# Kernel optimization log

Hardware: AMD Instinct MI355X
Metric: run time of the kernel (lower is better)

Reference implementation:

```python
import jax, jax.numpy as jnp
import numpy as np

D_MODEL = 512
N_EXPERTS = 8
TOPK = 2
D_FF = D_MODEL * 4
LB_WEIGHT = 0.01


def setup_inputs() -> dict:
    key = jax.random.key(0)
    k_x, k_g, k_w1, k_v1, k_w2 = jax.random.split(key, 5)
    B, L = 4, 2048
    x = jax.random.normal(k_x, (B, L, D_MODEL), dtype=jnp.float32)
    # nn.Linear gate weight, init std=0.01, shape [n_experts, d_model]
    gate_w = 0.01 * jax.random.normal(k_g, (N_EXPERTS, D_MODEL), dtype=jnp.float32)
    # kaiming_normal_ fan_in / relu: std = sqrt(2 / fan_in); fan_in is last dim
    std1 = np.sqrt(2.0 / D_MODEL).astype(np.float32)
    std2 = np.sqrt(2.0 / D_FF).astype(np.float32)
    W1 = std1 * jax.random.normal(k_w1, (N_EXPERTS, D_FF, D_MODEL), dtype=jnp.float32)
    V1 = std1 * jax.random.normal(k_v1, (N_EXPERTS, D_FF, D_MODEL), dtype=jnp.float32)
    W2 = std2 * jax.random.normal(k_w2, (N_EXPERTS, D_MODEL, D_FF), dtype=jnp.float32)
    return {"x": x, "gate_w": gate_w, "W1": W1, "V1": V1, "W2": W2}


def reference(x, gate_w, W1, V1, W2):
    B, L, D = x.shape
    T = B * L
    x_flat = x.reshape(T, D)

    # --- gating ---
    logits = x_flat @ gate_w.T                      # [T, E]
    probs = jax.nn.softmax(logits, axis=-1)         # [T, E]
    scores, indices = jax.lax.top_k(probs, TOPK)    # [T, K] each

    # combine weights: [T, E]; top-k indices per token are distinct
    oh = jax.nn.one_hot(indices, N_EXPERTS, dtype=x.dtype)    # [T, K, E]
    combine = jnp.einsum('tke,tk->te', oh, scores)            # [T, E]

    # load-balancing aux loss
    load = oh.sum(axis=(0, 1))                      # [E] tokens routed per expert
    f = load / T
    P = probs.mean(axis=0)                          # [E]
    aux_loss = N_EXPERTS * jnp.sum(f * P) * LB_WEIGHT

    # --- SwiGLU experts (dense over experts, masked combine) ---
    h = jnp.einsum('td,efd->etf', x_flat, W1)       # [E, T, d_ff]
    v = jnp.einsum('td,efd->etf', x_flat, V1)       # [E, T, d_ff]
    y = jnp.einsum('etf,edf->etd', jax.nn.silu(h) * v, W2)   # [E, T, D]

    out = jnp.einsum('te,etd->td', combine, y).reshape(B, L, D)
    return out, aux_loss
```

## Files before the change

kernel.cpp:

```cpp
#include <hip/hip_runtime.h>
#include <hip/hip_bf16.h>
#include <stdint.h>

#define D_MODEL 512
#define N_EXP 8
#define D_FF 2048
#define NTOK 8192
#define TM 256
#define MAX_TILES 72
#define NEPAD (MAX_TILES*TM)
#define BK 64

typedef __attribute__((ext_vector_type(8))) short short8;
typedef __attribute__((ext_vector_type(4))) float f32x4;

struct Ctrl {
  int cnt[8];
  int cursor[8];
  int offpad[16];
  int ntiles;
  int pad[3];
  int texp[MAX_TILES];
};

__device__ __forceinline__ unsigned short f2bf(float f){
  unsigned u = __float_as_uint(f);
  u += 0x7FFFu + ((u>>16)&1u);
  return (unsigned short)(u>>16);
}
__device__ __forceinline__ float bf2f(unsigned short v){
  return __uint_as_float(((unsigned)v)<<16);
}

__device__ __forceinline__ short8 pack8(float4 a, float4 b){
  short8 o;
  o[0]=(short)f2bf(a.x); o[1]=(short)f2bf(a.y); o[2]=(short)f2bf(a.z); o[3]=(short)f2bf(a.w);
  o[4]=(short)f2bf(b.x); o[5]=(short)f2bf(b.y); o[6]=(short)f2bf(b.z); o[7]=(short)f2bf(b.w);
  return o;
}

__device__ __forceinline__ void gload16(const void* g, void* l){
  __builtin_amdgcn_global_load_lds((const __attribute__((address_space(1))) unsigned int*)g,
                                   (__attribute__((address_space(3))) unsigned int*)l, 16, 0, 0);
}

#define SBAR0 __builtin_amdgcn_sched_barrier(0)
#define BAR   do{ SBAR0; __builtin_amdgcn_s_barrier(); SBAR0; }while(0)
#define LGKM0 do{ asm volatile("s_waitcnt lgkmcnt(0)" ::: "memory"); SBAR0; }while(0)
#define VM(N) do{ asm volatile("s_waitcnt vmcnt(" #N ")" ::: "memory"); SBAR0; }while(0)

__global__ void __launch_bounds__(256)
prep_kernel(const float* __restrict__ x, const float* __restrict__ gw,
            const float* __restrict__ W1, const float* __restrict__ V1, const float* __restrict__ W2,
            unsigned short* __restrict__ W1b, unsigned short* __restrict__ V1b, unsigned short* __restrict__ W2d,
            int* __restrict__ tok_e, float* __restrict__ tok_s,
            Ctrl* __restrict__ c, float* __restrict__ Pbins,
            unsigned short* __restrict__ Xb){
  __shared__ float gws[N_EXP*D_MODEL];
  __shared__ float pblk[4][8];
  __shared__ int cblk[8];
  int bid = blockIdx.x;
  int tid = threadIdx.x;
  if(bid >= 2048){
    int j = bid - 2048;
    const float* src = (j<4096) ? W1 : (j<8192 ? V1 : W2);
    unsigned short* dst = (j<4096) ? W1b : (j<8192 ? V1b : W2d);
    int i = (j & 4095)*2048 + tid*8;
    float4 a = *(const float4*)(src+i);
    float4 b = *(const float4*)(src+i+4);
    *(short8*)(dst+i) = pack8(a,b);
    return;
  }
  for(int i=tid; i<N_EXP*D_MODEL; i+=256) gws[i]=gw[i];
  if(tid<8) cblk[tid]=0;
  __syncthreads();
  int wave = tid>>6, lane = tid&63;
  int t = bid*4 + wave;
  const float* xr = x + (size_t)t*D_MODEL + lane*8;
  float4 xa = *(const float4*)xr;
  float4 xb = *(const float4*)(xr+4);
  *(short8*)(Xb + (size_t)t*D_MODEL + lane*8) = pack8(xa,xb);
  float le[8];
  #pragma unroll
  for(int e=0;e<8;e++){
    const float* g = gws + e*D_MODEL + lane*8;
    float4 ga = *(const float4*)g;
    float4 gb = *(const float4*)(g+4);
    le[e] = xa.x*ga.x + xa.y*ga.y + xa.z*ga.z + xa.w*ga.w
          + xb.x*gb.x + xb.y*gb.y + xb.z*gb.z + xb.w*gb.w;
  }
  #pragma unroll
  for(int e=0;e<8;e++){
    float v = le[e];
    #pragma unroll
    for(int off=1; off<64; off<<=1) v += __shfl_xor(v, off);
    le[e]=v;
  }
  float mx = le[0];
  #pragma unroll
  for(int e=1;e<8;e++) mx = fmaxf(mx, le[e]);
  float p[8], s=0.f;
  #pragma unroll
  for(int e=0;e<8;e++){ p[e]=__expf(le[e]-mx); s+=p[e]; }
  float inv = 1.0f/s;
  #pragma unroll
  for(int e=0;e<8;e++) p[e]*=inv;
  int e0=0; float s0=p[0];
  #pragma unroll
  for(int e=1;e<8;e++) if(p[e]>s0){e0=e;s0=p[e];}
  int e1=-1; float s1=-1.f;
  #pragma unroll
  for(int e=0;e<8;e++) if(e!=e0 && p[e]>s1){e1=e;s1=p[e];}
  if(lane==0){
    tok_e[2*t]=e0; tok_e[2*t+1]=e1;
    tok_s[2*t]=s0; tok_s[2*t+1]=s1;
    atomicAdd(&cblk[e0],1); atomicAdd(&cblk[e1],1);
    #pragma unroll
    for(int e=0;e<8;e++) pblk[wave][e]=p[e];
  }
  __syncthreads();
  if(tid<8){
    atomicAdd(&c->cnt[tid], cblk[tid]);
    atomicAdd(&Pbins[(bid&63)*8 + tid],
              pblk[0][tid]+pblk[1][tid]+pblk[2][tid]+pblk[3][tid]);
  }
}

__global__ void __launch_bounds__(256)
cvt_kernel(const float* __restrict__ src, unsigned short* __restrict__ dst, int n){
  int i = (blockIdx.x*256 + threadIdx.x)*8;
  if(i >= n) return;
  float4 a = *(const float4*)(src+i);
  float4 b = *(const float4*)(src+i+4);
  *(short8*)(dst+i) = pack8(a,b);
}

__global__ void __launch_bounds__(256)
scan_kernel(Ctrl* __restrict__ c, const float* __restrict__ Pbins, float* __restrict__ out){
  __shared__ float pred[4][8];
  int tid = threadIdx.x;
  float v = Pbins[tid] + Pbins[tid+256];
  v += __shfl_xor(v, 8);
  v += __shfl_xor(v, 16);
  v += __shfl_xor(v, 32);
  if((tid&63)<8) pred[tid>>6][tid&7] = v;
  __syncthreads();
  if(tid==0){
    int o=0, tc=0;
    float aux=0.f;
    for(int e=0;e<8;e++){
      float tot = pred[0][e]+pred[1][e]+pred[2][e]+pred[3][e];
      c->offpad[e]=o;
      int nt = (c->cnt[e]+TM-1)/TM;
      for(int i=0;i<nt;i++) c->texp[tc++]=e;
      o += nt*TM;
      c->cursor[e]=0;
      aux += ((float)c->cnt[e]/(float)NTOK) * (tot/(float)NTOK);
    }
    c->offpad[8]=o;
    c->ntiles=tc;
    out[(size_t)NTOK*D_MODEL] = 8.0f*0.01f*aux;
  }
}

__global__ void __launch_bounds__(256)
scatter_kernel(const int* __restrict__ tok_e, const float* __restrict__ tok_s,
               Ctrl* __restrict__ c, int* __restrict__ etok, float* __restrict__ escl,
               int* __restrict__ pos){
  int t = blockIdx.x*256 + threadIdx.x;
  if(t >= NTOK) return;
  #pragma unroll
  for(int k=0;k<2;k++){
    int e = tok_e[2*t+k];
    int p = atomicAdd(&c->cursor[e],1);
    int i = c->offpad[e]+p;
    etok[i]=t; escl[i]=tok_s[2*t+k];
    pos[2*t+k]=i;
  }
}

__global__ void __launch_bounds__(512,2)
expA_kernel(const unsigned short* __restrict__ Xb, const unsigned short* __restrict__ W1b,
            const unsigned short* __restrict__ V1b, const int* __restrict__ etok,
            const Ctrl* __restrict__ c, unsigned short* __restrict__ G){
  __shared__ short8 As[2][2048];
  __shared__ short8 Bs[2][2048];
  int bid = blockIdx.x;
  int chunk = bid & 7;
  int w_in = bid >> 3;
  int fb = w_in / 9;
  int tile = chunk*9 + (w_in - fb*9);
  int fbase = fb * 128;
  if(tile >= c->ntiles) return;
  int e = c->texp[tile];
  int base = tile*TM;
  int tid = threadIdx.x;

  int r0 = tid>>3;
  int cs = (tid&7) ^ (r0&7);
  int t0 = etok[base + r0];
  int t1 = etok[base + 64 + r0];
  int t2 = etok[base + 128 + r0];
  int t3 = etok[base + 192 + r0];
  const unsigned short* sA0 = Xb + (size_t)t0*D_MODEL + cs*8;
  const unsigned short* sA1 = Xb + (size_t)t1*D_MODEL + cs*8;
  const unsigned short* sA2 = Xb + (size_t)t2*D_MODEL + cs*8;
  const unsigned short* sA3 = Xb + (size_t)t3*D_MODEL + cs*8;
  const unsigned short* WE = W1b + (size_t)e*(D_FF*D_MODEL);
  const unsigned short* VE = V1b + (size_t)e*(D_FF*D_MODEL);
  const unsigned short* sB0 = WE + (size_t)(fbase+r0)*D_MODEL + cs*8;
  const unsigned short* sB1 = WE + (size_t)(fbase+64+r0)*D_MODEL + cs*8;
  const unsigned short* sB2 = VE + (size_t)(fbase+r0)*D_MODEL + cs*8;
  const unsigned short* sB3 = VE + (size_t)(fbase+64+r0)*D_MODEL + cs*8;
  int w64 = tid & ~63;

  int lane = tid&63, lrow = lane&15, lk = lane>>4;
  int wid = tid>>6, wr = wid>>2, wc = wid&3;
  int sw = lrow&7;
  int ch0 = lk ^ sw;
  int ch1 = (4+lk) ^ sw;

  f32x4 hacc[8][2], vacc[8][2];
  #pragma unroll
  for(int mi=0;mi<8;mi++)
    #pragma unroll
    for(int nj=0;nj<2;nj++){
      hacc[mi][nj]=(f32x4){0.f,0.f,0.f,0.f};
      vacc[mi][nj]=(f32x4){0.f,0.f,0.f,0.f};
    }

  auto ST_A0 = [&](int b, int kt){ size_t o=(size_t)kt*BK; gload16(sA0+o, &As[b][w64]);      gload16(sA1+o, &As[b][512+w64]); };
  auto ST_A1 = [&](int b, int kt){ size_t o=(size_t)kt*BK; gload16(sA2+o, &As[b][1024+w64]); gload16(sA3+o, &As[b][1536+w64]); };
  auto ST_W  = [&](int b, int kt){ size_t o=(size_t)kt*BK; gload16(sB0+o, &Bs[b][w64]);      gload16(sB1+o, &Bs[b][512+w64]); };
  auto ST_V  = [&](int b, int kt){ size_t o=(size_t)kt*BK; gload16(sB2+o, &Bs[b][1024+w64]); gload16(sB3+o, &Bs[b][1536+w64]); };

  ST_A0(0,0); ST_A1(0,0); ST_W(0,0); ST_V(0,0);
  ST_W(1,1); ST_V(1,1); ST_A0(1,1);
  VM(6);
  BAR;

  short8 alo[4][2], ahi[4][2], bw[2][2], bv[2][2];

  #pragma unroll
  for(int k=0;k<8;k++){
    const int cur = k&1, nxt = cur^1;
    #pragma unroll
    for(int j=0;j<4;j++){
      int s = (wr*128 + j*16 + lrow)*8;
      alo[j][0] = As[cur][s + ch0];
      alo[j][1] = As[cur][s + ch1];
    }
    #pragma unroll
    for(int nj=0;nj<2;nj++){
      int s = (wc*32 + nj*16 + lrow)*8;
      bw[nj][0] = Bs[cur][s + ch0];
      bw[nj][1] = Bs[cur][s + ch1];
    }
    if(k<7) ST_A1(nxt, k+1);
    BAR; LGKM0;
    __builtin_amdgcn_s_setprio(1);
    #pragma unroll
    for(int j=0;j<4;j++)
      #pragma unroll
      for(int nj=0;nj<2;nj++){
        hacc[j][nj] = __builtin_amdgcn_mfma_f32_16x16x32_bf16(alo[j][0], bw[nj][0], hacc[j][nj],0,0,0);
        hacc[j][nj] = __builtin_amdgcn_mfma_f32_16x16x32_bf16(alo[j][1], bw[nj][1], hacc[j][nj],0,0,0);
      }
    __builtin_amdgcn_s_setprio(0);
    BAR;
    #pragma unroll
    for(int nj=0;nj<2;nj++){
      int s = 1024 + (wc*32 + nj*16 + lrow)*8;
      bv[nj][0] = Bs[cur][s + ch0];
      bv[nj][1] = Bs[cur][s + ch1];
    }
    if(k<6) ST_W(cur, k+2);
    BAR; LGKM0;
    __builtin_amdgcn_s_setprio(1);
    #pragma unroll
    for(int j=0;j<4;j++)
      #pragma unroll
      for(int nj=0;nj<2;nj++){
        vacc[j][nj] = __builtin_amdgcn_mfma_f32_16x16x32_bf16(alo[j][0], bv[nj][0], vacc[j][nj],0,0,0);
        vacc[j][nj] = __builtin_amdgcn_mfma_f32_16x16x32_bf16(alo[j][1], bv[nj][1], vacc[j][nj],0,0,0);
      }
    __builtin_amdgcn_s_setprio(0);
    BAR;
    #pragma unroll
    for(int j=0;j<4;j++){
      int s = (wr*128 + 64 + j*16 + lrow)*8;
      ahi[j][0] = As[cur][s + ch0];
      ahi[j][1] = As[cur][s + ch1];
    }
    if(k<6) ST_V(cur, k+2);
    BAR; LGKM0;
    __builtin_amdgcn_s_setprio(1);
    #pragma unroll
    for(int j=0;j<4;j++)
      #pragma unroll
      for(int nj=0;nj<2;nj++){
        vacc[4+j][nj] = __builtin_amdgcn_mfma_f32_16x16x32_bf16(ahi[j][0], bv[nj][0], vacc[4+j][nj],0,0,0);
        vacc[4+j][nj] = __builtin_amdgcn_mfma_f32_16x16x32_bf16(ahi[j][1], bv[nj][1], vacc[4+j][nj],0,0,0);
      }
    __builtin_amdgcn_s_setprio(0);
    BAR;
    if(k<6) ST_A0(cur, k+2);
    if(k<6){ VM(6); } else { VM(0); }
    BAR;
    __builtin_amdgcn_s_setprio(1);
    #pragma unroll
    for(int j=0;j<4;j++)
      #pragma unroll
      for(int nj=0;nj<2;nj++){
        hacc[4+j][nj] = __builtin_amdgcn_mfma_f32_16x16x32_bf16(ahi[j][0], bw[nj][0], hacc[4+j][nj],0,0,0);
        hacc[4+j][nj] = __builtin_amdgcn_mfma_f32_16x16x32_bf16(ahi[j][1], bw[nj][1], hacc[4+j][nj],0,0,0);
      }
    __builtin_amdgcn_s_setprio(0);
    BAR;
  }

  #pragma unroll
  for(int mi=0;mi<8;mi++){
    int m = base + wr*128 + mi*16 + lk*4;
    #pragma unroll
    for(int nj=0;nj<2;nj++){
      int f = fbase + wc*32 + nj*16 + lrow;
      #pragma unroll
      for(int r=0;r<4;r++){
        float h = hacc[mi][nj][r], vv = vacc[mi][nj][r];
        float g = (h/(1.0f+__expf(-h)))*vv;
        G[(size_t)(m+r)*D_FF + f] = f2bf(g);
      }
    }
  }
}

__global__ void __launch_bounds__(512,2)
expB_kernel(const unsigned short* __restrict__ G, const unsigned short* __restrict__ W2b,
            const Ctrl* __restrict__ c, unsigned short* __restrict__ Ye){
  __shared__ short8 As2[2][2048];
  __shared__ short8 Bs2[2][2048];
  int bid = blockIdx.x;
  int w = (bid & 7)*18 + (bid >> 3);
  int tile = w >> 1;
  int nb = w & 1;
  if(tile >= c->ntiles) return;
  int e = c->texp[tile];
  int base = tile*TM;
  int nbase = nb*256;
  int tid = threadIdx.x;

  int r0 = tid>>3;
  int cs = (tid&7) ^ (r0&7);
  const unsigned short* sA0 = G + (size_t)(base+r0)*D_FF + cs*8;
  const unsigned short* sA1 = G + (size_t)(base+64+r0)*D_FF + cs*8;
  const unsigned short* sA2 = G + (size_t)(base+128+r0)*D_FF + cs*8;
  const unsigned short* sA3 = G + (size_t)(base+192+r0)*D_FF + cs*8;
  const unsigned short* W2E = W2b + (size_t)e*(D_MODEL*D_FF);
  const unsigned short* sB0 = W2E + (size_t)(nbase+r0)*D_FF + cs*8;
  const unsigned short* sB1 = W2E + (size_t)(nbase+64+r0)*D_FF + cs*8;
  const unsigned short* sB2 = W2E + (size_t)(nbase+128+r0)*D_FF + cs*8;
  const unsigned short* sB3 = W2E + (size_t)(nbase+192+r0)*D_FF + cs*8;
  int w64 = tid & ~63;

  int lane = tid&63, lrow = lane&15, lk = lane>>4;
  int wid = tid>>6, wr = wid>>2, wc = wid&3;
  int sw = lrow&7;
  int ch0 = lk ^ sw;
  int ch1 = (4+lk) ^ sw;

  f32x4 acc[8][4];
  #pragma unroll
  for(int mi=0;mi<8;mi++)
    #pragma unroll
    for(int nj=0;nj<4;nj++) acc[mi][nj]=(f32x4){0.f,0.f,0.f,0.f};

  auto ST_A0 = [&](int b, int kt){ size_t o=(size_t)kt*BK; gload16(sA0+o, &As2[b][w64]);      gload16(sA1+o, &As2[b][512+w64]); };
  auto ST_A1 = [&](int b, int kt){ size_t o=(size_t)kt*BK; gload16(sA2+o, &As2[b][1024+w64]); gload16(sA3+o, &As2[b][1536+w64]); };
  auto ST_B0 = [&](int b, int kt){ size_t o=(size_t)kt*BK; gload16(sB0+o, &Bs2[b][w64]);      gload16(sB1+o, &Bs2[b][512+w64]); };
  auto ST_B1 = [&](int b, int kt){ size_t o=(size_t)kt*BK; gload16(sB2+o, &Bs2[b][1024+w64]); gload16(sB3+o, &Bs2[b][1536+w64]); };

  ST_B0(0,0); ST_B1(0,0); ST_A0(0,0); ST_A1(0,0);
  ST_B0(1,1); ST_B1(1,1);
  VM(4);
  BAR;

  short8 alo[4][2], ahi[4][2], bl[2][2], bh[2][2];

  #pragma unroll 2
  for(int k=0;k<32;k++){
    const int cur = k&1, nxt = cur^1;
    #pragma unroll
    for(int j=0;j<4;j++){
      int s = (wr*128 + j*16 + lrow)*8;
      alo[j][0] = As2[cur][s + ch0];
      alo[j][1] = As2[cur][s + ch1];
    }
    #pragma unroll
    for(int nj=0;nj<2;nj++){
      int s = (wc*64 + nj*16 + lrow)*8;
      bl[nj][0] = Bs2[cur][s + ch0];
      bl[nj][1] = Bs2[cur][s + ch1];
    }
    if(k<31) ST_A0(nxt, k+1);
    BAR; LGKM0;
    __builtin_amdgcn_s_setprio(1);
    #pragma unroll
    for(int j=0;j<4;j++)
      #pragma unroll
      for(int nj=0;nj<2;nj++){
        acc[j][nj] = __builtin_amdgcn_mfma_f32_16x16x32_bf16(alo[j][0], bl[nj][0], acc[j][nj],0,0,0);
        acc[j][nj] = __builtin_amdgcn_mfma_f32_16x16x32_bf16(alo[j][1], bl[nj][1], acc[j][nj],0,0,0);
      }
    __builtin_amdgcn_s_setprio(0);
    BAR;
    #pragma unroll
    for(int nj=0;nj<2;nj++){
      int s = (wc*64 + 32 + nj*16 + lrow)*8;
      bh[nj][0] = Bs2[cur][s + ch0];
      bh[nj][1] = Bs2[cur][s + ch1];
    }
    if(k<31) ST_A1(nxt, k+1);
    BAR; LGKM0;
    __builtin_amdgcn_s_setprio(1);
    #pragma unroll
    for(int j=0;j<4;j++)
      #pragma unroll
      for(int nj=0;nj<2;nj++){
        acc[j][2+nj] = __builtin_amdgcn_mfma_f32_16x16x32_bf16(alo[j][0], bh[nj][0], acc[j][2+nj],0,0,0);
        acc[j][2+nj] = __builtin_amdgcn_mfma_f32_16x16x32_bf16(alo[j][1], bh[nj][1], acc[j][2+nj],0,0,0);
      }
    __builtin_amdgcn_s_setprio(0);
    BAR;
    #pragma unroll
    for(int j=0;j<4;j++){
      int s = (wr*128 + 64 + j*16 + lrow)*8;
      ahi[j][0] = As2[cur][s + ch0];
      ahi[j][1] = As2[cur][s + ch1];
    }
    if(k<30) ST_B0(cur, k+2);
    BAR; LGKM0;
    __builtin_amdgcn_s_setprio(1);
    #pragma unroll
    for(int j=0;j<4;j++)
      #pragma unroll
      for(int nj=0;nj<2;nj++){
        acc[4+j][2+nj] = __builtin_amdgcn_mfma_f32_16x16x32_bf16(ahi[j][0], bh[nj][0], acc[4+j][2+nj],0,0,0);
        acc[4+j][2+nj] = __builtin_amdgcn_mfma_f32_16x16x32_bf16(ahi[j][1], bh[nj][1], acc[4+j][2+nj],0,0,0);
      }
    __builtin_amdgcn_s_setprio(0);
    BAR;
    if(k<30) ST_B1(cur, k+2);
    if(k<30){ VM(4); } else { VM(0); }
    BAR;
    __builtin_amdgcn_s_setprio(1);
    #pragma unroll
    for(int j=0;j<4;j++)
      #pragma unroll
      for(int nj=0;nj<2;nj++){
        acc[4+j][nj] = __builtin_amdgcn_mfma_f32_16x16x32_bf16(ahi[j][0], bl[nj][0], acc[4+j][nj],0,0,0);
        acc[4+j][nj] = __builtin_amdgcn_mfma_f32_16x16x32_bf16(ahi[j][1], bl[nj][1], acc[4+j][nj],0,0,0);
      }
    __builtin_amdgcn_s_setprio(0);
    BAR;
  }

  #pragma unroll
  for(int mi=0;mi<8;mi++){
    #pragma unroll
    for(int r=0;r<4;r++){
      int m = base + wr*128 + mi*16 + lk*4 + r;
      #pragma unroll
      for(int nj=0;nj<4;nj++){
        int n = nbase + wc*64 + nj*16 + lrow;
        Ye[(size_t)m*D_MODEL + n] = f2bf(acc[mi][nj][r]);
      }
    }
  }
}

__global__ void __launch_bounds__(256)
combine_kernel(const unsigned short* __restrict__ Ye, const int* __restrict__ pos,
               const float* __restrict__ tok_s, float* __restrict__ out){
  int wave = threadIdx.x>>6, lane = threadIdx.x&63;
  int t = blockIdx.x*4 + wave;
  int p0 = pos[2*t], p1 = pos[2*t+1];
  float s0 = tok_s[2*t], s1 = tok_s[2*t+1];
  short8 y0 = *(const short8*)(Ye + (size_t)p0*D_MODEL + lane*8);
  short8 y1 = *(const short8*)(Ye + (size_t)p1*D_MODEL + lane*8);
  float* o = out + (size_t)t*D_MODEL + lane*8;
  float v[8];
  #pragma unroll
  for(int i=0;i<8;i++)
    v[i] = s0*bf2f((unsigned short)y0[i]) + s1*bf2f((unsigned short)y1[i]);
  float4 lo = {v[0],v[1],v[2],v[3]};
  float4 hi = {v[4],v[5],v[6],v[7]};
  *(float4*)o = lo;
  *(float4*)(o+4) = hi;
}

extern "C" void kernel_launch(void* const* d_in, const int* in_sizes, int n_in,
                              void* d_out, int out_size, void* d_ws, size_t ws_size,
                              hipStream_t stream) {
  (void)in_sizes; (void)n_in; (void)out_size;
  const float* x  = (const float*)d_in[0];
  const float* gw = (const float*)d_in[1];
  const float* W1 = (const float*)d_in[2];
  const float* V1 = (const float*)d_in[3];
  const float* W2 = (const float*)d_in[4];
  float* out = (float*)d_out;

  const size_t WSZ = (size_t)N_EXP*D_FF*D_MODEL;
  const size_t XSZ = (size_t)NTOK*D_MODEL;
  char* ws = (char*)d_ws;
  size_t off = 0;
  unsigned short* W1b = (unsigned short*)(ws+off); off += WSZ*2;
  unsigned short* V1b = (unsigned short*)(ws+off); size_t v1_off = off; off += WSZ*2;
  unsigned short* Xb  = (unsigned short*)(ws+off); off += XSZ*2;
  unsigned short* G   = (unsigned short*)(ws+off); off += (size_t)NEPAD*D_FF*2;
  int*   etok  = (int*)(ws+off);   size_t entry_off = off; off += (size_t)NEPAD*4;
  float* escl  = (float*)(ws+off); off += (size_t)NEPAD*4;
  size_t entry_bytes = off - entry_off;
  int*   pos   = (int*)(ws+off);   off += (size_t)NTOK*2*4;
  int*   tok_e = (int*)(ws+off);   off += (size_t)NTOK*2*4;
  float* tok_s = (float*)(ws+off); off += (size_t)NTOK*2*4;
  float* Pbins = (float*)(ws+off); size_t pb_off = off; off += 512*4;
  Ctrl*  ctrl  = (Ctrl*)(ws+off);  off += sizeof(Ctrl);
  size_t pb_bytes = off - pb_off;
  unsigned short* Ye  = (unsigned short*)(ws+v1_off);
  if(ws_size < off) return;

  unsigned short* W2d = (unsigned short*)(ws+off);
  bool hoistW2 = (ws_size >= off + WSZ*2);
  unsigned short* W2b = hoistW2 ? W2d : W1b;

  hipMemsetAsync(ws+entry_off, 0, entry_bytes, stream);
  hipMemsetAsync(ws+pb_off, 0, pb_bytes, stream);

  int nconv = hoistW2 ? 3 : 2;
  prep_kernel<<<2048 + nconv*4096, 256, 0, stream>>>(x, gw, W1, V1, W2, W1b, V1b, W2d,
                                                     tok_e, tok_s, ctrl, Pbins, Xb);
  scan_kernel<<<1, 256, 0, stream>>>(ctrl, Pbins, out);
  scatter_kernel<<<NTOK/256, 256, 0, stream>>>(tok_e, tok_s, ctrl, etok, escl, pos);

  expA_kernel<<<1152, 512, 0, stream>>>(Xb, W1b, V1b, etok, ctrl, G);
  if(!hoistW2)
    cvt_kernel<<<(int)WSZ/(256*8), 256, 0, stream>>>(W2, W1b, (int)WSZ);
  expB_kernel<<<144, 512, 0, stream>>>(G, W2b, ctrl, Ye);
  combine_kernel<<<NTOK/4, 256, 0, stream>>>(Ye, pos, tok_s, out);
}
```

Baseline: 316.2 us.

## Merge scan into scatter, drop entry memset, restructure GEMM prefetch to one stage per iteration

Folds the single-block scan kernel into the scatter kernel: every block recomputes the padded per-expert offsets locally, and block 0 writes the tile map and the aux loss. The memset of etok/escl is removed, and expA masks token indices with NTOK-1 so that uninitialised padding rows still point at valid memory. In both expert GEMMs the four staggered partial loads per K-step, each with its own barrier, become a single combined prefetch issued mid-iteration, which cuts most of the barriers. Risks: the cursor relies on being zeroed elsewhere, since the scan no longer resets it; the per-expert tile map (texp, ntiles) is now written by block 0 of the same kernel without any cross-block sync; and the new pipeline waits longer on the prefetch.

```diff
diff --git a/kernel.cpp b/kernel.cpp
--- a/kernel.cpp
+++ b/kernel.cpp
@@ -136,46 +136,50 @@
 }
 
 __global__ void __launch_bounds__(256)
-scan_kernel(Ctrl* __restrict__ c, const float* __restrict__ Pbins, float* __restrict__ out){
+scatter_kernel(const int* __restrict__ tok_e, const float* __restrict__ tok_s,
+               Ctrl* __restrict__ c, int* __restrict__ etok, float* __restrict__ escl,
+               int* __restrict__ pos, const float* __restrict__ Pbins, float* __restrict__ out){
+  __shared__ int soff[8];
   __shared__ float pred[4][8];
   int tid = threadIdx.x;
-  float v = Pbins[tid] + Pbins[tid+256];
-  v += __shfl_xor(v, 8);
-  v += __shfl_xor(v, 16);
-  v += __shfl_xor(v, 32);
-  if((tid&63)<8) pred[tid>>6][tid&7] = v;
+  if(tid==0){
+    int o=0;
+    #pragma unroll
+    for(int e=0;e<8;e++){ soff[e]=o; o += ((c->cnt[e]+TM-1)/TM)*TM; }
+  }
   __syncthreads();
-  if(tid==0){
-    int o=0, tc=0;
-    float aux=0.f;
-    for(int e=0;e<8;e++){
-      float tot = pred[0][e]+pred[1][e]+pred[2][e]+pred[3][e];
-      c->offpad[e]=o;
-      int nt = (c->cnt[e]+TM-1)/TM;
-      for(int i=0;i<nt;i++) c->texp[tc++]=e;
-      o += nt*TM;
-      c->cursor[e]=0;
-      aux += ((float)c->cnt[e]/(float)NTOK) * (tot/(float)NTOK);
-    }
-    c->offpad[8]=o;
-    c->ntiles=tc;
-    out[(size_t)NTOK*D_MODEL] = 8.0f*0.01f*aux;
-  }
-}
-
-__global__ void __launch_bounds__(256)
-scatter_kernel(const int* __restrict__ tok_e, const float* __restrict__ tok_s,
-               Ctrl* __restrict__ c, int* __restrict__ etok, float* __restrict__ escl,
-               int* __restrict__ pos){
-  int t = blockIdx.x*256 + threadIdx.x;
-  if(t >= NTOK) return;
+  int t = blockIdx.x*256 + tid;
   #pragma unroll
   for(int k=0;k<2;k++){
     int e = tok_e[2*t+k];
     int p = atomicAdd(&c->cursor[e],1);
-    int i = c->offpad[e]+p;
+    int i = soff[e]+p;
     etok[i]=t; escl[i]=tok_s[2*t+k];
     pos[2*t+k]=i;
+  }
+  if(blockIdx.x==0){
+    float v = Pbins[tid] + Pbins[tid+256];
+    v += __shfl_xor(v, 8);
+    v += __shfl_xor(v, 16);
+    v += __shfl_xor(v, 32);
+    if((tid&63)<8) pred[tid>>6][tid&7] = v;
+    __syncthreads();
+    if(tid==0){
+      int o=0, tc=0;
+      float aux=0.f;
+      #pragma unroll
+      for(int e=0;e<8;e++){
+        float tot = pred[0][e]+pred[1][e]+pred[2][e]+pred[3][e];
+        c->offpad[e]=o;
+        int nt = (c->cnt[e]+TM-1)/TM;
+        for(int i=0;i<nt;i++) c->texp[tc++]=e;
+        o += nt*TM;
+        aux += ((float)c->cnt[e]/(float)NTOK) * (tot/(float)NTOK);
+      }
+      c->offpad[8]=o;
+      c->ntiles=tc;
+      out[(size_t)NTOK*D_MODEL] = 8.0f*0.01f*aux;
+    }
   }
 }
 
@@ -198,10 +202,10 @@
 
   int r0 = tid>>3;
   int cs = (tid&7) ^ (r0&7);
-  int t0 = etok[base + r0];
-  int t1 = etok[base + 64 + r0];
-  int t2 = etok[base + 128 + r0];
-  int t3 = etok[base + 192 + r0];
+  int t0 = etok[base + r0] & (NTOK-1);
+  int t1 = etok[base + 64 + r0] & (NTOK-1);
+  int t2 = etok[base + 128 + r0] & (NTOK-1);
+  int t3 = etok[base + 192 + r0] & (NTOK-1);
   const unsigned short* sA0 = Xb + (size_t)t0*D_MODEL + cs*8;
   const unsigned short* sA1 = Xb + (size_t)t1*D_MODEL + cs*8;
   const unsigned short* sA2 = Xb + (size_t)t2*D_MODEL + cs*8;
@@ -229,21 +233,24 @@
       vacc[mi][nj]=(f32x4){0.f,0.f,0.f,0.f};
     }
 
-  auto ST_A0 = [&](int b, int kt){ size_t o=(size_t)kt*BK; gload16(sA0+o, &As[b][w64]);      gload16(sA1+o, &As[b][512+w64]); };
-  auto ST_A1 = [&](int b, int kt){ size_t o=(size_t)kt*BK; gload16(sA2+o, &As[b][1024+w64]); gload16(sA3+o, &As[b][1536+w64]); };
-  auto ST_W  = [&](int b, int kt){ size_t o=(size_t)kt*BK; gload16(sB0+o, &Bs[b][w64]);      gload16(sB1+o, &Bs[b][512+w64]); };
-  auto ST_V  = [&](int b, int kt){ size_t o=(size_t)kt*BK; gload16(sB2+o, &Bs[b][1024+w64]); gload16(sB3+o, &Bs[b][1536+w64]); };
-
-  ST_A0(0,0); ST_A1(0,0); ST_W(0,0); ST_V(0,0);
-  ST_W(1,1); ST_V(1,1); ST_A0(1,1);
-  VM(6);
+  auto ST_ALL = [&](int b, int kt){
+    size_t o=(size_t)kt*BK;
+    gload16(sA0+o, &As[b][w64]);      gload16(sA1+o, &As[b][512+w64]);
+    gload16(sA2+o, &As[b][1024+w64]); gload16(sA3+o, &As[b][1536+w64]);
+    gload16(sB0+o, &Bs[b][w64]);      gload16(sB1+o, &Bs[b][512+w64]);
+    gload16(sB2+o, &Bs[b][1024+w64]); gload16(sB3+o, &Bs[b][1536+w64]);
+  };
+
+  ST_ALL(0,0);
+  ST_ALL(1,1);
+  VM(8);
   BAR;
 
   short8 alo[4][2], ahi[4][2], bw[2][2], bv[2][2];
 
   #pragma unroll
   for(int k=0;k<8;k++){
-    const int cur = k&1, nxt = cur^1;
+    const int cur = k&1;
     #pragma unroll
     for(int j=0;j<4;j++){
       int s = (wr*128 + j*16 + lrow)*8;
@@ -256,8 +263,6 @@
       bw[nj][0] = Bs[cur][s + ch0];
       bw[nj][1] = Bs[cur][s + ch1];
     }
-    if(k<7) ST_A1(nxt, k+1);
-    BAR; LGKM0;
     __builtin_amdgcn_s_setprio(1);
     #pragma unroll
     for(int j=0;j<4;j++)
@@ -267,15 +272,12 @@
         hacc[j][nj] = __builtin_amdgcn_mfma_f32_16x16x32_bf16(alo[j][1], bw[nj][1], hacc[j][nj],0,0,0);
       }
     __builtin_amdgcn_s_setprio(0);
-    BAR;
     #pragma unroll
     for(int nj=0;nj<2;nj++){
       int s = 1024 + (wc*32 + nj*16 + lrow)*8;
       bv[nj][0] = Bs[cur][s + ch0];
       bv[nj][1] = Bs[cur][s + ch1];
     }
-    if(k<6) ST_W(cur, k+2);
-    BAR; LGKM0;
     __builtin_amdgcn_s_setprio(1);
     #pragma unroll
     for(int j=0;j<4;j++)
@@ -285,15 +287,12 @@
         vacc[j][nj] = __builtin_amdgcn_mfma_f32_16x16x32_bf16(alo[j][1], bv[nj][1], vacc[j][nj],0,0,0);
       }
     __builtin_amdgcn_s_setprio(0);
-    BAR;
     #pragma unroll
     for(int j=0;j<4;j++){
       int s = (wr*128 + 64 + j*16 + lrow)*8;
       ahi[j][0] = As[cur][s + ch0];
       ahi[j][1] = As[cur][s + ch1];
     }
-    if(k<6) ST_V(cur, k+2);
-    BAR; LGKM0;
     __builtin_amdgcn_s_setprio(1);
     #pragma unroll
     for(int j=0;j<4;j++)
@@ -303,10 +302,9 @@
         vacc[4+j][nj] = __builtin_amdgcn_mfma_f32_16x16x32_bf16(ahi[j][1], bv[nj][1], vacc[4+j][nj],0,0,0);
       }
     __builtin_amdgcn_s_setprio(0);
+    LGKM0;
     BAR;
-    if(k<6) ST_A0(cur, k+2);
-    if(k<6){ VM(6); } else { VM(0); }
-    BAR;
+    if(k<6) ST_ALL(cur, k+2);
     __builtin_amdgcn_s_setprio(1);
     #pragma unroll
     for(int j=0;j<4;j++)
@@ -316,6 +314,7 @@
         hacc[4+j][nj] = __builtin_amdgcn_mfma_f32_16x16x32_bf16(ahi[j][1], bw[nj][1], hacc[4+j][nj],0,0,0);
       }
     __builtin_amdgcn_s_setprio(0);
+    if(k<6){ VM(8); } else if(k==6){ VM(0); }
     BAR;
   }
 
@@ -375,21 +374,24 @@
     #pragma unroll
     for(int nj=0;nj<4;nj++) acc[mi][nj]=(f32x4){0.f,0.f,0.f,0.f};
 
-  auto ST_A0 = [&](int b, int kt){ size_t o=(size_t)kt*BK; gload16(sA0+o, &As2[b][w64]);      gload16(sA1+o, &As2[b][512+w64]); };
-  auto ST_A1 = [&](int b, int kt){ size_t o=(size_t)kt*BK; gload16(sA2+o, &As2[b][1024+w64]); gload16(sA3+o, &As2[b][1536+w64]); };
-  auto ST_B0 = [&](int b, int kt){ size_t o=(size_t)kt*BK; gload16(sB0+o, &Bs2[b][w64]);      gload16(sB1+o, &Bs2[b][512+w64]); };
-  auto ST_B1 = [&](int b, int kt){ size_t o=(size_t)kt*BK; gload16(sB2+o, &Bs2[b][1024+w64]); gload16(sB3+o, &Bs2[b][1536+w64]); };
-
-  ST_B0(0,0); ST_B1(0,0); ST_A0(0,0); ST_A1(0,0);
-  ST_B0(1,1); ST_B1(1,1);
-  VM(4);
+  auto ST_ALL = [&](int b, int kt){
+    size_t o=(size_t)kt*BK;
+    gload16(sA0+o, &As2[b][w64]);      gload16(sA1+o, &As2[b][512+w64]);
+    gload16(sA2+o, &As2[b][1024+w64]); gload16(sA3+o, &As2[b][1536+w64]);
+    gload16(sB0+o, &Bs2[b][w64]);      gload16(sB1+o, &Bs2[b][512+w64]);
+    gload16(sB2+o, &Bs2[b][1024+w64]); gload16(sB3+o, &Bs2[b][1536+w64]);
+  };
+
+  ST_ALL(0,0);
+  ST_ALL(1,1);
+  VM(8);
   BAR;
 
   short8 alo[4][2], ahi[4][2], bl[2][2], bh[2][2];
 
   #pragma unroll 2
   for(int k=0;k<32;k++){
-    const int cur = k&1, nxt = cur^1;
+    const int cur = k&1;
     #pragma unroll
     for(int j=0;j<4;j++){
       int s = (wr*128 + j*16 + lrow)*8;
@@ -402,8 +404,6 @@
       bl[nj][0] = Bs2[cur][s + ch0];
       bl[nj][1] = Bs2[cur][s + ch1];
     }
-    if(k<31) ST_A0(nxt, k+1);
-    BAR; LGKM0;
     __builtin_amdgcn_s_setprio(1);
     #pragma unroll
     for(int j=0;j<4;j++)
@@ -413,15 +413,12 @@
         acc[j][nj] = __builtin_amdgcn_mfma_f32_16x16x32_bf16(alo[j][1], bl[nj][1], acc[j][nj],0,0,0);
       }
     __builtin_amdgcn_s_setprio(0);
-    BAR;
     #pragma unroll
     for(int nj=0;nj<2;nj++){
       int s = (wc*64 + 32 + nj*16 + lrow)*8;
       bh[nj][0] = Bs2[cur][s + ch0];
       bh[nj][1] = Bs2[cur][s + ch1];
     }
-    if(k<31) ST_A1(nxt, k+1);
-    BAR; LGKM0;
     __builtin_amdgcn_s_setprio(1);
     #pragma unroll
     for(int j=0;j<4;j++)
@@ -431,15 +428,12 @@
         acc[j][2+nj] = __builtin_amdgcn_mfma_f32_16x16x32_bf16(alo[j][1], bh[nj][1], acc[j][2+nj],0,0,0);
       }
     __builtin_amdgcn_s_setprio(0);
-    BAR;
     #pragma unroll
     for(int j=0;j<4;j++){
       int s = (wr*128 + 64 + j*16 + lrow)*8;
       ahi[j][0] = As2[cur][s + ch0];
       ahi[j][1] = As2[cur][s + ch1];
     }
-    if(k<30) ST_B0(cur, k+2);
-    BAR; LGKM0;
     __builtin_amdgcn_s_setprio(1);
     #pragma unroll
     for(int j=0;j<4;j++)
@@ -449,10 +443,9 @@
         acc[4+j][2+nj] = __builtin_amdgcn_mfma_f32_16x16x32_bf16(ahi[j][1], bh[nj][1], acc[4+j][2+nj],0,0,0);
       }
     __builtin_amdgcn_s_setprio(0);
+    LGKM0;
     BAR;
-    if(k<30) ST_B1(cur, k+2);
-    if(k<30){ VM(4); } else { VM(0); }
-    BAR;
+    if(k<30) ST_ALL(cur, k+2);
     __builtin_amdgcn_s_setprio(1);
     #pragma unroll
     for(int j=0;j<4;j++)
@@ -462,6 +455,7 @@
         acc[4+j][nj] = __builtin_amdgcn_mfma_f32_16x16x32_bf16(ahi[j][1], bl[nj][1], acc[4+j][nj],0,0,0);
       }
     __builtin_amdgcn_s_setprio(0);
+    if(k<30){ VM(8); } else if(k==30){ VM(0); }
     BAR;
   }
 
@@ -518,9 +512,8 @@
   unsigned short* V1b = (unsigned short*)(ws+off); size_t v1_off = off; off += WSZ*2;
   unsigned short* Xb  = (unsigned short*)(ws+off); off += XSZ*2;
   unsigned short* G   = (unsigned short*)(ws+off); off += (size_t)NEPAD*D_FF*2;
-  int*   etok  = (int*)(ws+off);   size_t entry_off = off; off += (size_t)NEPAD*4;
+  int*   etok  = (int*)(ws+off);   off += (size_t)NEPAD*4;
   float* escl  = (float*)(ws+off); off += (size_t)NEPAD*4;
-  size_t entry_bytes = off - entry_off;
   int*   pos   = (int*)(ws+off);   off += (size_t)NTOK*2*4;
   int*   tok_e = (int*)(ws+off);   off += (size_t)NTOK*2*4;
   float* tok_s = (float*)(ws+off); off += (size_t)NTOK*2*4;
@@ -534,14 +527,12 @@
   bool hoistW2 = (ws_size >= off + WSZ*2);
   unsigned short* W2b = hoistW2 ? W2d : W1b;
 
-  hipMemsetAsync(ws+entry_off, 0, entry_bytes, stream);
   hipMemsetAsync(ws+pb_off, 0, pb_bytes, stream);
 
   int nconv = hoistW2 ? 3 : 2;
   prep_kernel<<<2048 + nconv*4096, 256, 0, stream>>>(x, gw, W1, V1, W2, W1b, V1b, W2d,
                                                      tok_e, tok_s, ctrl, Pbins, Xb);
-  scan_kernel<<<1, 256, 0, stream>>>(ctrl, Pbins, out);
-  scatter_kernel<<<NTOK/256, 256, 0, stream>>>(tok_e, tok_s, ctrl, etok, escl, pos);
+  scatter_kernel<<<NTOK/256, 256, 0, stream>>>(tok_e, tok_s, ctrl, etok, escl, pos, Pbins, out);
 
   expA_kernel<<<1152, 512, 0, stream>>>(Xb, W1b, V1b, etok, ctrl, G);
   if(!hoistW2)
```

After: 280.5 us. -11.3%, faster.
